# Kernel tuning notes

Hardware: AMD Instinct MI355X
Metric: run time of the kernel (lower is better)

## Reference

```python
import jax, jax.numpy as jnp
import numpy as np


def _l2norm(t, eps=1e-12):
    # matches torch F.normalize(p=2, dim=-1): x / max(||x||_2, eps)
    n = jnp.sqrt(jnp.sum(t * t, axis=-1, keepdims=True))
    return t / jnp.maximum(n, eps)


def setup_inputs() -> dict:
    key = jax.random.key(0)
    ks = jax.random.split(key, 8)
    B, N, C, H, W = 16, 4, 256, 64, 64
    d = 64  # dim_head
    x = jax.random.normal(ks[0], (B, C, H, W), jnp.float32)
    fmaps = jax.random.normal(ks[1], (B, N, C, H, W), jnp.float32)
    Wq = jax.random.normal(ks[2], (N * d, C), jnp.float32) * 0.02   # Linear [out,in]
    Wk = jax.random.normal(ks[3], (N, d, C), jnp.float32) * 0.02    # grouped 1x1 conv, per-group [d,C]
    Wv = jax.random.normal(ks[4], (N, d, C), jnp.float32) * 0.02
    rescale = jnp.ones((N, 1, 1), jnp.float32)
    Wffn = jax.random.normal(ks[5], (C, N * d), jnp.float32) * 0.02
    bffn = jnp.zeros((C,), jnp.float32)
    return {"x": x, "fmaps": fmaps, "Wq": Wq, "Wk": Wk, "Wv": Wv,
            "rescale": rescale, "Wffn": Wffn, "bffn": bffn}


def reference(x, fmaps, Wq, Wk, Wv, rescale, Wffn, bffn):
    B, N, C, H, W = fmaps.shape
    d = Wk.shape[1]
    HW = H * W

    # x: [B,C,H,W] -> tokens [B,HW,C]
    x_in = jnp.transpose(x, (0, 2, 3, 1)).reshape(B, HW, C)
    q_in = jnp.einsum('bsc,oc->bso', x_in, Wq)            # [B,HW,N*d]

    # grouped 1x1 convs on fmaps (group = fmap index n)
    fm = fmaps.reshape(B, N, C, HW)                       # [B,N,C,HW]
    k = jnp.einsum('bncs,ndc->bnds', fm, Wk)              # [B,N,d,HW]
    v = jnp.einsum('bncs,ndc->bnds', fm, Wv)              # [B,N,d,HW]

    q = jnp.transpose(q_in.reshape(B, HW, N, d), (0, 2, 3, 1))  # [B,N,d,HW]

    qn = _l2norm(q)   # normalize over spatial (HW) axis
    kn = _l2norm(k)

    attn = jnp.einsum('bnds,bnes->bnde', kn, qn) * rescale      # [B,N,d,d]
    attn = jax.nn.softmax(attn, axis=-1)
    out = jnp.einsum('bnde,bnes->bnds', attn, v)                # [B,N,d,HW]

    out = jnp.transpose(out, (0, 3, 1, 2)).reshape(B, HW, N * d)  # [B,HW,N*d]
    out = out + q_in
    out = jnp.einsum('bsi,ci->bsc', out, Wffn) + bffn + q_in      # ffn + residual
    return jnp.transpose(out.reshape(B, H, W, C), (0, 3, 1, 2))   # [B,C,H,W]
```

## Files before the change

kernel.cpp:

```cpp
#include <hip/hip_runtime.h>
#include <hip/hip_bf16.h>
#include <cmath>

using bf16 = __hip_bfloat16;
typedef __attribute__((ext_vector_type(4))) float  f32x4;
typedef __attribute__((ext_vector_type(8))) short  bf16x8;
typedef unsigned int u32;
typedef unsigned short u16;

__device__ __forceinline__ void gl_lds16(const bf16* g, bf16* l) {
    __builtin_amdgcn_global_load_lds(
        (const __attribute__((address_space(1))) u32*)g,
        (__attribute__((address_space(3))) u32*)l, 16, 0, 0);
}

__device__ __forceinline__ u32 pk2(float a, float b) {
    bf16 ha = __float2bfloat16(a), hb = __float2bfloat16(b);
    return (u32)*(u16*)&ha | ((u32)*(u16*)&hb << 16);
}
__device__ __forceinline__ float b2f(u16 v) {
    return __uint_as_float((u32)v << 16);
}

__global__ __launch_bounds__(512) void qproj8(
    const float* __restrict__ x,
    const bf16* __restrict__ Wq,
    bf16* __restrict__ qch)
{
    __shared__ __align__(16) bf16 sW[256 * 64];
    __shared__ __align__(16) bf16 sX[128 * 72];
    const int t = threadIdx.x;
    const int lane = t & 63, wid = t >> 6;
    const int wm = wid >> 1, wn = wid & 1;
    const int g = lane >> 4, lr = lane & 15;
    const int s0 = blockIdx.x * 128;
    const int b = blockIdx.y;
    const float* xb = x + (long)b * 1048576;

    f32x4 acc[4][4];
#pragma unroll
    for (int i = 0; i < 4; ++i)
#pragma unroll
        for (int j = 0; j < 4; ++j) acc[i][j] = (f32x4){0.f, 0.f, 0.f, 0.f};

    const int p  = t & 31;
    const int sl = t >> 5;

    for (int c0 = 0; c0 < 256; c0 += 64) {
        __syncthreads();
#pragma unroll
        for (int i = 0; i < 4; ++i) {
            int lin = i * 512 + t, r = lin >> 3, ch = lin & 7;
            gl_lds16(Wq + (long)r * 256 + c0 + ((ch ^ (r & 7)) << 3), &sW[lin * 8]);
        }
#pragma unroll
        for (int j = 0; j < 2; ++j) {
            int s4 = j * 16 + sl;
            const float* src = xb + (long)(c0 + 2 * p) * 4096 + s0 + s4 * 4;
            float4 a = *(const float4*)src;
            float4 bq = *(const float4*)(src + 4096);
            char* base = (char*)sX + p * 4 + (s4 * 4) * 144;
            *(u32*)(base +   0) = pk2(a.x, bq.x);
            *(u32*)(base + 144) = pk2(a.y, bq.y);
            *(u32*)(base + 288) = pk2(a.z, bq.z);
            *(u32*)(base + 432) = pk2(a.w, bq.w);
        }
        __syncthreads();
#pragma unroll
        for (int kk = 0; kk < 2; ++kk) {
            bf16x8 aw[4], fx[4];
#pragma unroll
            for (int mf = 0; mf < 4; ++mf) {
                int r = wm * 64 + mf * 16 + lr;
                aw[mf] = *(const bf16x8*)((const char*)sW + r * 128 + (((kk * 4 + g) ^ (r & 7)) << 4));
            }
#pragma unroll
            for (int nf = 0; nf < 4; ++nf) {
                int s = wn * 64 + nf * 16 + lr;
                fx[nf] = *(const bf16x8*)((const char*)sX + s * 144 + (kk * 4 + g) * 16);
            }
#pragma unroll
            for (int mf = 0; mf < 4; ++mf)
#pragma unroll
                for (int nf = 0; nf < 4; ++nf)
                    acc[mf][nf] = __builtin_amdgcn_mfma_f32_16x16x32_bf16(
                        aw[mf], fx[nf], acc[mf][nf], 0, 0, 0);
        }
    }
    bf16* qb = qch + (long)b * 1048576;
#pragma unroll
    for (int mf = 0; mf < 4; ++mf)
#pragma unroll
        for (int nf = 0; nf < 4; ++nf)
#pragma unroll
            for (int e = 0; e < 4; ++e) {
                int o = wm * 64 + mf * 16 + g * 4 + e;
                int s = s0 + wn * 64 + nf * 16 + lr;
                qb[(long)o * 4096 + s] = __float2bfloat16(acc[mf][nf][e]);
            }
}

__global__ __launch_bounds__(256) void kvproj(
    const float* __restrict__ fm,
    const bf16* __restrict__ Wk,
    const bf16* __restrict__ Wv,
    bf16* __restrict__ kb,
    bf16* __restrict__ vT)
{
    __shared__ bf16 sF[2][128 * 72];
    __shared__ bf16 sK[2][64 * 64];
    __shared__ bf16 sV[2][64 * 64];
    const int t = threadIdx.x;
    const int lane = t & 63, wid = t >> 6;
    const int g = lane >> 4, lr = lane & 15;
    const int s0 = blockIdx.x * 128;
    const int bn = blockIdx.y, n = bn & 3;
    const float* fb = fm + (long)bn * 1048576;
    const bf16* WkN = Wk + (long)n * 16384;
    const bf16* WvN = Wv + (long)n * 16384;

    f32x4 acc1[4][2];
    f32x4 acc2[2][4];
#pragma unroll
    for (int i = 0; i < 4; ++i)
#pragma unroll
        for (int j = 0; j < 2; ++j) {
            acc1[i][j] = (f32x4){0.f, 0.f, 0.f, 0.f};
            acc2[j][i] = (f32x4){0.f, 0.f, 0.f, 0.f};
        }

    const int p  = t & 31;
    const int sl = t >> 5;

    {
#pragma unroll
        for (int i = 0; i < 2; ++i) {
            int lin = i * 256 + t, r = lin >> 3, ch = lin & 7;
            int off = r * 256 + ((ch ^ (r & 7)) << 3);
            gl_lds16(WkN + off, &sK[0][lin * 8]);
            gl_lds16(WvN + off, &sV[0][lin * 8]);
        }
        float4 ra[4], rb[4];
#pragma unroll
        for (int j = 0; j < 4; ++j) {
            const float* src = fb + (long)(2 * p) * 4096 + s0 + (j * 8 + sl) * 4;
            ra[j] = *(const float4*)src;
            rb[j] = *(const float4*)(src + 4096);
        }
#pragma unroll
        for (int j = 0; j < 4; ++j) {
            char* base = (char*)&sF[0][0] + p * 4 + ((j * 8 + sl) * 4) * 144;
            *(u32*)(base +   0) = pk2(ra[j].x, rb[j].x);
            *(u32*)(base + 144) = pk2(ra[j].y, rb[j].y);
            *(u32*)(base + 288) = pk2(ra[j].z, rb[j].z);
            *(u32*)(base + 432) = pk2(ra[j].w, rb[j].w);
        }
        __syncthreads();
    }

    int cur = 0;
    for (int it = 0; it < 4; ++it) {
        const int c0n = (it + 1) * 64;
        float4 ra[4], rb[4];
        if (it < 3) {
#pragma unroll
            for (int i = 0; i < 2; ++i) {
                int lin = i * 256 + t, r = lin >> 3, ch = lin & 7;
                int off = r * 256 + c0n + ((ch ^ (r & 7)) << 3);
                gl_lds16(WkN + off, &sK[cur ^ 1][lin * 8]);
                gl_lds16(WvN + off, &sV[cur ^ 1][lin * 8]);
            }
#pragma unroll
            for (int j = 0; j < 4; ++j) {
                const float* src = fb + (long)(c0n + 2 * p) * 4096 + s0 + (j * 8 + sl) * 4;
                ra[j] = *(const float4*)src;
                rb[j] = *(const float4*)(src + 4096);
            }
        }
        const char* fbase = (const char*)&sF[cur][0];
        const char* kbase = (const char*)&sK[cur][0];
        const char* vbase = (const char*)&sV[cur][0];
#pragma unroll
        for (int kk = 0; kk < 2; ++kk) {
            bf16x8 ak[4], ff[2], bv[4];
#pragma unroll
            for (int mf = 0; mf < 4; ++mf) {
                int r = mf * 16 + lr;
                ak[mf] = *(const bf16x8*)(kbase + r * 128 + (((kk * 4 + g) ^ (r & 7)) << 4));
            }
#pragma unroll
            for (int i = 0; i < 2; ++i) {
                int s = wid * 32 + i * 16 + lr;
                ff[i] = *(const bf16x8*)(fbase + s * 144 + (kk * 4 + g) * 16);
            }
#pragma unroll
            for (int nf = 0; nf < 4; ++nf) {
                int r = nf * 16 + lr;
                bv[nf] = *(const bf16x8*)(vbase + r * 128 + (((kk * 4 + g) ^ (r & 7)) << 4));
            }
#pragma unroll
            for (int mf = 0; mf < 4; ++mf)
#pragma unroll
                for (int i = 0; i < 2; ++i)
                    acc1[mf][i] = __builtin_amdgcn_mfma_f32_16x16x32_bf16(
                        ak[mf], ff[i], acc1[mf][i], 0, 0, 0);
#pragma unroll
            for (int i = 0; i < 2; ++i)
#pragma unroll
                for (int nf = 0; nf < 4; ++nf)
                    acc2[i][nf] = __builtin_amdgcn_mfma_f32_16x16x32_bf16(
                        ff[i], bv[nf], acc2[i][nf], 0, 0, 0);
        }
        if (it < 3) {
#pragma unroll
            for (int j = 0; j < 4; ++j) {
                char* base = (char*)&sF[cur ^ 1][0] + p * 4 + ((j * 8 + sl) * 4) * 144;
                *(u32*)(base +   0) = pk2(ra[j].x, rb[j].x);
                *(u32*)(base + 144) = pk2(ra[j].y, rb[j].y);
                *(u32*)(base + 288) = pk2(ra[j].z, rb[j].z);
                *(u32*)(base + 432) = pk2(ra[j].w, rb[j].w);
            }
            __syncthreads();
            cur ^= 1;
        }
    }

    bf16* kbb = kb + (long)bn * 262144;
#pragma unroll
    for (int mf = 0; mf < 4; ++mf)
#pragma unroll
        for (int i = 0; i < 2; ++i)
#pragma unroll
            for (int e = 0; e < 4; ++e) {
                int dd = mf * 16 + g * 4 + e;
                int s  = s0 + wid * 32 + i * 16 + lr;
                kbb[(long)dd * 4096 + s] = __float2bfloat16(acc1[mf][i][e]);
            }
    bf16* vtb = vT + (long)bn * 262144;
#pragma unroll
    for (int i = 0; i < 2; ++i)
#pragma unroll
        for (int nf = 0; nf < 4; ++nf)
#pragma unroll
            for (int e = 0; e < 4; ++e) {
                int s = s0 + wid * 32 + i * 16 + g * 4 + e;
                int ec = nf * 16 + lr;
                vtb[(long)s * 64 + ec] = __float2bfloat16(acc2[i][nf][e]);
            }
}

__global__ __launch_bounds__(256) void qk_sum(
    const bf16* __restrict__ kb,
    const bf16* __restrict__ qch,
    float* __restrict__ part,
    float* __restrict__ sumq, float* __restrict__ sumk)
{
    __shared__ bf16 sA[2][64 * 64];
    __shared__ bf16 sB[2][64 * 64];
    const int t = threadIdx.x;
    const int lane = t & 63, wid = t >> 6;
    const int wm = wid >> 1, wn = wid & 1;
    const int g = lane >> 4, lr = lane & 15;
    const int ch_ = blockIdx.x;
    const int bn = blockIdx.y;
    const bf16* kbase = kb + (long)bn * 262144;
    const bf16* qbase = qch + (long)bn * 262144;

    const int srow = t >> 1;
    const int shalf = t & 1;

    f32x4 acc[2][2];
#pragma unroll
    for (int i = 0; i < 2; ++i)
#pragma unroll
        for (int j = 0; j < 2; ++j) acc[i][j] = (f32x4){0.f, 0.f, 0.f, 0.f};
    float ss = 0.f;

    {
        int k0 = ch_ * 512;
#pragma unroll
        for (int i = 0; i < 2; ++i) {
            int lin = i * 256 + t, r = lin >> 3, c = lin & 7;
            gl_lds16(kbase + (long)r * 4096 + k0 + ((c ^ (r & 7)) << 3), &sA[0][lin * 8]);
            gl_lds16(qbase + (long)r * 4096 + k0 + ((c ^ (r & 7)) << 3), &sB[0][lin * 8]);
        }
        __syncthreads();
    }

    int cur = 0;
    for (int it = 0; it < 8; ++it) {
        if (it < 7) {
            int k0 = ch_ * 512 + (it + 1) * 64;
#pragma unroll
            for (int i = 0; i < 2; ++i) {
                int lin = i * 256 + t, r = lin >> 3, c = lin & 7;
                gl_lds16(kbase + (long)r * 4096 + k0 + ((c ^ (r & 7)) << 3), &sA[cur ^ 1][lin * 8]);
                gl_lds16(qbase + (long)r * 4096 + k0 + ((c ^ (r & 7)) << 3), &sB[cur ^ 1][lin * 8]);
            }
        }
        const char* abase = (const char*)&sA[cur][0];
        const char* bbase = (const char*)&sB[cur][0];
#pragma unroll
        for (int kk = 0; kk < 2; ++kk) {
            bf16x8 af[2], bf[2];
#pragma unroll
            for (int mf = 0; mf < 2; ++mf) {
                int r = wm * 32 + mf * 16 + lr;
                af[mf] = *(const bf16x8*)(abase + r * 128 + (((kk * 4 + g) ^ (r & 7)) << 4));
            }
#pragma unroll
            for (int nf = 0; nf < 2; ++nf) {
                int r = wn * 32 + nf * 16 + lr;
                bf[nf] = *(const bf16x8*)(bbase + r * 128 + (((kk * 4 + g) ^ (r & 7)) << 4));
            }
#pragma unroll
            for (int mf = 0; mf < 2; ++mf)
#pragma unroll
                for (int nf = 0; nf < 2; ++nf)
                    acc[mf][nf] = __builtin_amdgcn_mfma_f32_16x16x32_bf16(
                        af[mf], bf[nf], acc[mf][nf], 0, 0, 0);
        }
        {
            const char* base = (srow < 64) ? abase + srow * 128
                                           : bbase + (srow - 64) * 128;
            int r7 = srow & 7;
#pragma unroll
            for (int j = 0; j < 4; ++j) {
                bf16x8 v = *(const bf16x8*)(base + (((shalf * 4 + j) ^ r7) << 4));
#pragma unroll
                for (int e = 0; e < 8; ++e) {
                    float f = b2f((u16)v[e]);
                    ss += f * f;
                }
            }
        }
        __syncthreads();
        cur ^= 1;
    }

    ss += __shfl_xor(ss, 1);
    if (shalf == 0) {
        if (srow < 64) sumk[ch_ * 4096 + bn * 64 + srow] = ss;
        else           sumq[ch_ * 4096 + bn * 64 + srow - 64] = ss;
    }
    float* pp = part + ((long)bn * 8 + ch_) * 4096;
#pragma unroll
    for (int mf = 0; mf < 2; ++mf)
#pragma unroll
        for (int nf = 0; nf < 2; ++nf)
#pragma unroll
            for (int e = 0; e < 4; ++e) {
                int m = wm * 32 + mf * 16 + g * 4 + e;
                int nn = wn * 32 + nf * 16 + lr;
                pp[m * 64 + nn] = acc[mf][nf][e];
            }
}

__global__ __launch_bounds__(256) void attn_finalize_kernel(
    const float* __restrict__ part,
    const float* __restrict__ sumq, const float* __restrict__ sumk,
    const float* __restrict__ rescale,
    bf16* __restrict__ attn_out)
{
    const int bn = blockIdx.x;
    const int n = bn & 3;
    const int t = threadIdx.x;
    const float rs = rescale[n];

    __shared__ float att[64][65];
    __shared__ float rmax[64], rsum[64];
    __shared__ float iq[64], ik[64];

    if (t < 64) {
        float s = 0.f;
#pragma unroll
        for (int c = 0; c < 8; ++c) s += sumk[c * 4096 + bn * 64 + t];
        ik[t] = 1.f / fmaxf(sqrtf(s), 1e-12f);
    } else if (t < 128) {
        float s = 0.f;
#pragma unroll
        for (int c = 0; c < 8; ++c) s += sumq[c * 4096 + bn * 64 + t - 64];
        iq[t - 64] = 1.f / fmaxf(sqrtf(s), 1e-12f);
    }
    __syncthreads();

    const float* pb = part + (size_t)bn * 8 * 4096;
#pragma unroll
    for (int p = 0; p < 16; ++p) {
        int lin = p * 256 + t;
        int dd = lin >> 6, e = lin & 63;
        float v = 0.f;
#pragma unroll
        for (int c = 0; c < 8; ++c) v += pb[c * 4096 + lin];
        v *= ik[dd] * iq[e] * rs;
        att[dd][e] = v;
    }
    __syncthreads();
    if (t < 64) {
        float m = -1e30f;
        for (int e = 0; e < 64; ++e) m = fmaxf(m, att[t][e]);
        float sm = 0.f;
        for (int e = 0; e < 64; ++e) sm += expf(att[t][e] - m);
        rmax[t] = m;
        rsum[t] = 1.0f / sm;
    }
    __syncthreads();
    bf16* ob = attn_out + (size_t)bn * 4096;
#pragma unroll
    for (int p = 0; p < 16; ++p) {
        int lin = p * 256 + t;
        int dd = lin >> 6, e = lin & 63;
        ob[lin] = __float2bfloat16(expf(att[dd][e] - rmax[dd]) * rsum[dd]);
    }
}

__global__ __launch_bounds__(256) void pvffn(
    const bf16* __restrict__ vT,
    const bf16* __restrict__ attnb,
    const bf16* __restrict__ qch,
    const bf16* __restrict__ Wf,
    const float* __restrict__ bffn,
    float* __restrict__ out)
{
    __shared__ bf16 bufA[2][8192];
    __shared__ bf16 Zs[64 * 64];
    const int t = threadIdx.x;
    const int lane = t & 63, wid = t >> 6;
    const int g = lane >> 4, lr = lane & 15;
    const int s0 = blockIdx.x * 64;
    const int b = blockIdx.y;

    f32x4 accF[4][4];
#pragma unroll
    for (int i = 0; i < 4; ++i)
#pragma unroll
        for (int j = 0; j < 4; ++j) accF[i][j] = (f32x4){0.f, 0.f, 0.f, 0.f};

    {
        const int bn = b * 4;
#pragma unroll
        for (int i = 0; i < 2; ++i) {
            int lin = i * 256 + t, r = lin >> 3, c = lin & 7;
            gl_lds16(vT + (long)bn * 262144 + (long)(s0 + r) * 64 + ((c ^ (r & 7)) << 3),
                     &bufA[0][lin * 8]);
            gl_lds16(attnb + (long)bn * 4096 + r * 64 + ((c ^ (r & 7)) << 3),
                     &bufA[0][4096 + lin * 8]);
        }
        __syncthreads();
    }

    for (int n = 0; n < 4; ++n) {
        const int bn = b * 4 + n;
        const int cur = n & 1;
        if (n < 3) {
            const int bnn = bn + 1;
#pragma unroll
            for (int i = 0; i < 2; ++i) {
                int lin = i * 256 + t, r = lin >> 3, c = lin & 7;
                gl_lds16(vT + (long)bnn * 262144 + (long)(s0 + r) * 64 + ((c ^ (r & 7)) << 3),
                         &bufA[cur ^ 1][lin * 8]);
                gl_lds16(attnb + (long)bnn * 4096 + r * 64 + ((c ^ (r & 7)) << 3),
                         &bufA[cur ^ 1][4096 + lin * 8]);
            }
        }
        bf16x8 wf[2][4];
#pragma unroll
        for (int kk = 0; kk < 2; ++kk)
#pragma unroll
            for (int mf = 0; mf < 4; ++mf)
                wf[kk][mf] = *(const bf16x8*)(
                    Wf + (long)(wid * 64 + mf * 16 + lr) * 256 + n * 64 + (kk * 4 + g) * 8);

        const char* vb = (const char*)&bufA[cur][0];
        const char* ab = vb + 8192;
        f32x4 accP[4];
#pragma unroll
        for (int j = 0; j < 4; ++j) accP[j] = (f32x4){0.f, 0.f, 0.f, 0.f};
#pragma unroll
        for (int kk = 0; kk < 2; ++kk) {
            int r = wid * 16 + lr;
            bf16x8 av = *(const bf16x8*)(vb + r * 128 + (((kk * 4 + g) ^ (r & 7)) << 4));
            bf16x8 at[4];
#pragma unroll
            for (int nf = 0; nf < 4; ++nf) {
                int rr = nf * 16 + lr;
                at[nf] = *(const bf16x8*)(ab + rr * 128 + (((kk * 4 + g) ^ (rr & 7)) << 4));
            }
#pragma unroll
            for (int nf = 0; nf < 4; ++nf)
                accP[nf] = __builtin_amdgcn_mfma_f32_16x16x32_bf16(
                    av, at[nf], accP[nf], 0, 0, 0);
        }
#pragma unroll
        for (int nf = 0; nf < 4; ++nf) {
            int slb = wid * 16 + g * 4;
            int il = nf * 16 + lr;
            ushort4 qv = *(const ushort4*)(qch + ((long)b * 256 + n * 64 + il) * 4096 + s0 + slb);
            u16 qa[4] = {qv.x, qv.y, qv.z, qv.w};
#pragma unroll
            for (int e = 0; e < 4; ++e) {
                int sl = slb + e;
                float v = accP[nf][e] + b2f(qa[e]);
                bf16 hv = __float2bfloat16(v);
                int byte = sl * 128 + ((((il >> 3) ^ (sl & 7))) << 4) + (il & 7) * 2;
                *(u16*)((char*)Zs + byte) = *(u16*)&hv;
            }
        }
        __syncthreads();
#pragma unroll
        for (int kk = 0; kk < 2; ++kk) {
            bf16x8 bz[4];
#pragma unroll
            for (int nf = 0; nf < 4; ++nf) {
                int sl = nf * 16 + lr;
                bz[nf] = *(const bf16x8*)((const char*)Zs + sl * 128 + (((kk * 4 + g) ^ (sl & 7)) << 4));
            }
#pragma unroll
            for (int mf = 0; mf < 4; ++mf)
#pragma unroll
                for (int nf = 0; nf < 4; ++nf)
                    accF[mf][nf] = __builtin_amdgcn_mfma_f32_16x16x32_bf16(
                        wf[kk][mf], bz[nf], accF[mf][nf], 0, 0, 0);
        }
        __syncthreads();
    }

    float* ob = out + (long)b * 1048576;
    const bf16* qb = qch + (long)b * 1048576;
#pragma unroll
    for (int mf = 0; mf < 4; ++mf)
#pragma unroll
        for (int e = 0; e < 4; ++e) {
            int c = wid * 64 + mf * 16 + g * 4 + e;
            float bv = bffn[c];
#pragma unroll
            for (int nf = 0; nf < 4; ++nf) {
                int s = s0 + nf * 16 + lr;
                long idx = (long)c * 4096 + s;
                ob[idx] = accF[mf][nf][e] + bv + b2f(*(const u16*)(qb + idx));
            }
        }
}

__global__ __launch_bounds__(256) void wconv(
    const float* __restrict__ a, const float* __restrict__ b,
    const float* __restrict__ c, const float* __restrict__ d,
    bf16* __restrict__ o)
{
    int i = blockIdx.x * 256 + threadIdx.x;
    int which = i >> 16, off = i & 65535;
    const float* s = (which == 0) ? a : (which == 1) ? b : (which == 2) ? c : d;
    o[i] = __float2bfloat16(s[off]);
}

extern "C" void kernel_launch(void* const* d_in, const int* in_sizes, int n_in,
                              void* d_out, int out_size, void* d_ws, size_t ws_size,
                              hipStream_t stream) {
    const float* x       = (const float*)d_in[0];
    const float* fmaps   = (const float*)d_in[1];
    const float* Wq      = (const float*)d_in[2];
    const float* Wk      = (const float*)d_in[3];
    const float* Wv      = (const float*)d_in[4];
    const float* rescale = (const float*)d_in[5];
    const float* Wffn    = (const float*)d_in[6];
    const float* bffn    = (const float*)d_in[7];
    float* out = (float*)d_out;

    char* w = (char*)d_ws;
    bf16* kbuf  = (bf16*)(w + 0);
    bf16* vT    = (bf16*)(w + 33554432L);
    bf16* qch   = (bf16*)(w + 67108864L);
    float* part = (float*)(w + 100663296L);
    bf16* attnb = (bf16*)(w + 109051904L);
    float* sumq = (float*)(w + 109576192L);
    float* sumk = (float*)(w + 109707264L);
    bf16* Wq_b  = (bf16*)(w + 109838336L);
    bf16* Wk_b  = Wq_b + 65536;
    bf16* Wv_b  = Wq_b + 131072;
    bf16* Wf_b  = Wq_b + 196608;

    dim3 blk(256);

    wconv<<<dim3(1024), blk, 0, stream>>>(Wq, Wk, Wv, Wffn, Wq_b);
    kvproj<<<dim3(32, 64), blk, 0, stream>>>(fmaps, Wk_b, Wv_b, kbuf, vT);
    qproj8<<<dim3(32, 16), dim3(512), 0, stream>>>(x, Wq_b, qch);
    qk_sum<<<dim3(8, 64), blk, 0, stream>>>(kbuf, qch, part, sumq, sumk);
    attn_finalize_kernel<<<dim3(64), blk, 0, stream>>>(part, sumq, sumk, rescale, attnb);
    pvffn<<<dim3(64, 16), blk, 0, stream>>>(vT, attnb, qch, Wf_b, bffn, out);
}
```

Measured before the change: 180.1 us.

## Fuse K/V projection with K·Q partial reduction into one kernel

```diff
diff --git a/kernel.cpp b/kernel.cpp
--- a/kernel.cpp
+++ b/kernel.cpp
@@ -100,56 +100,60 @@
             }
 }
 
-__global__ __launch_bounds__(256) void kvproj(
+__global__ __launch_bounds__(256) void kvqk2(
     const float* __restrict__ fm,
     const bf16* __restrict__ Wk,
     const bf16* __restrict__ Wv,
-    bf16* __restrict__ kb,
-    bf16* __restrict__ vT)
+    const bf16* __restrict__ qch,
+    bf16* __restrict__ vT,
+    float* __restrict__ part,
+    float* __restrict__ sumq, float* __restrict__ sumk)
 {
-    __shared__ bf16 sF[2][128 * 72];
-    __shared__ bf16 sK[2][64 * 64];
-    __shared__ bf16 sV[2][64 * 64];
+    __shared__ __align__(16) char smem[69632];
+
     const int t = threadIdx.x;
     const int lane = t & 63, wid = t >> 6;
     const int g = lane >> 4, lr = lane & 15;
-    const int s0 = blockIdx.x * 128;
+    const int ch_ = blockIdx.x;
     const int bn = blockIdx.y, n = bn & 3;
     const float* fb = fm + (long)bn * 1048576;
     const bf16* WkN = Wk + (long)n * 16384;
     const bf16* WvN = Wv + (long)n * 16384;
-
-    f32x4 acc1[4][2];
-    f32x4 acc2[2][4];
-#pragma unroll
-    for (int i = 0; i < 4; ++i)
-#pragma unroll
-        for (int j = 0; j < 2; ++j) {
-            acc1[i][j] = (f32x4){0.f, 0.f, 0.f, 0.f};
-            acc2[j][i] = (f32x4){0.f, 0.f, 0.f, 0.f};
-        }
+    const bf16* qbase = qch + (long)bn * 262144;
+    bf16* vtb = vT + (long)bn * 262144;
 
     const int p  = t & 31;
     const int sl = t >> 5;
+
+    f32x4 accQ[4];
+#pragma unroll
+    for (int i = 0; i < 4; ++i) accQ[i] = (f32x4){0.f, 0.f, 0.f, 0.f};
+    float kss[4][4];
+#pragma unroll
+    for (int i = 0; i < 4; ++i)
+#pragma unroll
+        for (int j = 0; j < 4; ++j) kss[i][j] = 0.f;
+    float qss[4] = {0.f, 0.f, 0.f, 0.f};
 
     {
 #pragma unroll
         for (int i = 0; i < 2; ++i) {
             int lin = i * 256 + t, r = lin >> 3, ch = lin & 7;
             int off = r * 256 + ((ch ^ (r & 7)) << 3);
-            gl_lds16(WkN + off, &sK[0][lin * 8]);
-            gl_lds16(WvN + off, &sV[0][lin * 8]);
-        }
+            gl_lds16(WkN + off, (bf16*)(smem + 36864) + lin * 8);
+            gl_lds16(WvN + off, (bf16*)(smem + 53248) + lin * 8);
+        }
+        const int ss0 = ch_ * 512;
         float4 ra[4], rb[4];
 #pragma unroll
         for (int j = 0; j < 4; ++j) {
-            const float* src = fb + (long)(2 * p) * 4096 + s0 + (j * 8 + sl) * 4;
+            const float* src = fb + (long)(2 * p) * 4096 + ss0 + (j * 8 + sl) * 4;
             ra[j] = *(const float4*)src;
             rb[j] = *(const float4*)(src + 4096);
         }
 #pragma unroll
         for (int j = 0; j < 4; ++j) {
-            char* base = (char*)&sF[0][0] + p * 4 + ((j * 8 + sl) * 4) * 144;
+            char* base = smem + p * 4 + ((j * 8 + sl) * 4) * 144;
             *(u32*)(base +   0) = pk2(ra[j].x, rb[j].x);
             *(u32*)(base + 144) = pk2(ra[j].y, rb[j].y);
             *(u32*)(base + 288) = pk2(ra[j].z, rb[j].z);
@@ -158,202 +162,196 @@
         __syncthreads();
     }
 
-    int cur = 0;
-    for (int it = 0; it < 4; ++it) {
-        const int c0n = (it + 1) * 64;
-        float4 ra[4], rb[4];
-        if (it < 3) {
+    int fcur = 0, wcur = 0;
+    f32x4 acc1[4][2], acc2[2][4];
+
+    for (int fi = 0; fi < 16; ++fi) {
+        const int c = fi & 3;
+        if (c == 0) {
+#pragma unroll
+            for (int i = 0; i < 4; ++i)
+#pragma unroll
+                for (int j = 0; j < 2; ++j) {
+                    acc1[i][j] = (f32x4){0.f, 0.f, 0.f, 0.f};
+                    acc2[j][i] = (f32x4){0.f, 0.f, 0.f, 0.f};
+                }
+        }
+        const bool havF = (fi < 15);
+        if (c < 3) {
+            char* kw = (wcur ? smem + 36864 : smem + 45056);
+            char* vw = (wcur ? smem + 53248 : smem + 61440);
 #pragma unroll
             for (int i = 0; i < 2; ++i) {
                 int lin = i * 256 + t, r = lin >> 3, ch = lin & 7;
-                int off = r * 256 + c0n + ((ch ^ (r & 7)) << 3);
-                gl_lds16(WkN + off, &sK[cur ^ 1][lin * 8]);
-                gl_lds16(WvN + off, &sV[cur ^ 1][lin * 8]);
-            }
+                int off = r * 256 + (c + 1) * 64 + ((ch ^ (r & 7)) << 3);
+                gl_lds16(WkN + off, (bf16*)kw + lin * 8);
+                gl_lds16(WvN + off, (bf16*)vw + lin * 8);
+            }
+        }
+        float4 ra[4], rb[4];
+        if (havF) {
+            const int nss0 = ch_ * 512 + ((fi + 1) >> 2) * 128;
+            const int nc0  = ((fi + 1) & 3) * 64;
 #pragma unroll
             for (int j = 0; j < 4; ++j) {
-                const float* src = fb + (long)(c0n + 2 * p) * 4096 + s0 + (j * 8 + sl) * 4;
+                const float* src = fb + (long)(nc0 + 2 * p) * 4096 + nss0 + (j * 8 + sl) * 4;
                 ra[j] = *(const float4*)src;
                 rb[j] = *(const float4*)(src + 4096);
             }
         }
-        const char* fbase = (const char*)&sF[cur][0];
-        const char* kbase = (const char*)&sK[cur][0];
-        const char* vbase = (const char*)&sV[cur][0];
-#pragma unroll
-        for (int kk = 0; kk < 2; ++kk) {
-            bf16x8 ak[4], ff[2], bv[4];
-#pragma unroll
-            for (int mf = 0; mf < 4; ++mf) {
-                int r = mf * 16 + lr;
-                ak[mf] = *(const bf16x8*)(kbase + r * 128 + (((kk * 4 + g) ^ (r & 7)) << 4));
-            }
-#pragma unroll
-            for (int i = 0; i < 2; ++i) {
-                int s = wid * 32 + i * 16 + lr;
-                ff[i] = *(const bf16x8*)(fbase + s * 144 + (kk * 4 + g) * 16);
-            }
-#pragma unroll
-            for (int nf = 0; nf < 4; ++nf) {
-                int r = nf * 16 + lr;
-                bv[nf] = *(const bf16x8*)(vbase + r * 128 + (((kk * 4 + g) ^ (r & 7)) << 4));
-            }
-#pragma unroll
-            for (int mf = 0; mf < 4; ++mf)
+        {
+            const char* fbase = smem + (fcur ? 18432 : 0);
+            const char* kbase = smem + (wcur ? 45056 : 36864);
+            const char* vbase = smem + (wcur ? 61440 : 53248);
+#pragma unroll
+            for (int kk = 0; kk < 2; ++kk) {
+                bf16x8 ak[4], ff[2], bv[4];
+#pragma unroll
+                for (int mf = 0; mf < 4; ++mf) {
+                    int r = mf * 16 + lr;
+                    ak[mf] = *(const bf16x8*)(kbase + r * 128 + (((kk * 4 + g) ^ (r & 7)) << 4));
+                }
+#pragma unroll
+                for (int i = 0; i < 2; ++i) {
+                    int s = wid * 32 + i * 16 + lr;
+                    ff[i] = *(const bf16x8*)(fbase + s * 144 + (kk * 4 + g) * 16);
+                }
+#pragma unroll
+                for (int nf = 0; nf < 4; ++nf) {
+                    int r = nf * 16 + lr;
+                    bv[nf] = *(const bf16x8*)(vbase + r * 128 + (((kk * 4 + g) ^ (r & 7)) << 4));
+                }
+#pragma unroll
+                for (int mf = 0; mf < 4; ++mf)
+#pragma unroll
+                    for (int i = 0; i < 2; ++i)
+                        acc1[mf][i] = __builtin_amdgcn_mfma_f32_16x16x32_bf16(
+                            ak[mf], ff[i], acc1[mf][i], 0, 0, 0);
 #pragma unroll
                 for (int i = 0; i < 2; ++i)
-                    acc1[mf][i] = __builtin_amdgcn_mfma_f32_16x16x32_bf16(
-                        ak[mf], ff[i], acc1[mf][i], 0, 0, 0);
-#pragma unroll
-            for (int i = 0; i < 2; ++i)
-#pragma unroll
-                for (int nf = 0; nf < 4; ++nf)
-                    acc2[i][nf] = __builtin_amdgcn_mfma_f32_16x16x32_bf16(
-                        ff[i], bv[nf], acc2[i][nf], 0, 0, 0);
-        }
-        if (it < 3) {
+#pragma unroll
+                    for (int nf = 0; nf < 4; ++nf)
+                        acc2[i][nf] = __builtin_amdgcn_mfma_f32_16x16x32_bf16(
+                            ff[i], bv[nf], acc2[i][nf], 0, 0, 0);
+            }
+        }
+        if (havF) {
+            char* nb = smem + (fcur ? 0 : 18432);
 #pragma unroll
             for (int j = 0; j < 4; ++j) {
-                char* base = (char*)&sF[cur ^ 1][0] + p * 4 + ((j * 8 + sl) * 4) * 144;
+                char* base = nb + p * 4 + ((j * 8 + sl) * 4) * 144;
                 *(u32*)(base +   0) = pk2(ra[j].x, rb[j].x);
                 *(u32*)(base + 144) = pk2(ra[j].y, rb[j].y);
                 *(u32*)(base + 288) = pk2(ra[j].z, rb[j].z);
                 *(u32*)(base + 432) = pk2(ra[j].w, rb[j].w);
             }
             __syncthreads();
-            cur ^= 1;
-        }
-    }
-
-    bf16* kbb = kb + (long)bn * 262144;
-#pragma unroll
-    for (int mf = 0; mf < 4; ++mf)
-#pragma unroll
-        for (int i = 0; i < 2; ++i)
+            fcur ^= 1;
+        }
+        if (c < 3) wcur ^= 1;
+
+        if (c == 3) {
+            const int sub = fi >> 2;
+            const int ss0 = ch_ * 512 + sub * 128;
+            const int ovl = wcur ^ 1;
+            char* ktA = smem + (ovl ? 45056 : 36864);
+            char* ktB = smem + (ovl ? 61440 : 53248);
+#pragma unroll
+            for (int mf = 0; mf < 4; ++mf)
+#pragma unroll
+                for (int i = 0; i < 2; ++i)
+#pragma unroll
+                    for (int e = 0; e < 4; ++e) {
+                        int dd = mf * 16 + g * 4 + e;
+                        int sc = wid * 32 + i * 16 + lr;
+                        float f = acc1[mf][i][e];
+                        kss[mf][e] += f * f;
+                        bf16 hv = __float2bfloat16(f);
+                        char* base = (dd < 32) ? ktA : ktB;
+                        int byte = (dd & 31) * 256 + ((((sc >> 3) ^ (dd & 7))) << 4) + (sc & 7) * 2;
+                        *(u16*)(base + byte) = *(u16*)&hv;
+                    }
+            if (sub < 3) {
+                char* kw = (wcur ? smem + 45056 : smem + 36864);
+                char* vw = (wcur ? smem + 61440 : smem + 53248);
+#pragma unroll
+                for (int i = 0; i < 2; ++i) {
+                    int lin = i * 256 + t, r = lin >> 3, ch = lin & 7;
+                    int off = r * 256 + ((ch ^ (r & 7)) << 3);
+                    gl_lds16(WkN + off, (bf16*)kw + lin * 8);
+                    gl_lds16(WvN + off, (bf16*)vw + lin * 8);
+                }
+            }
+            __syncthreads();
+#pragma unroll
+            for (int kks = 0; kks < 4; ++kks) {
+                int rA = wid * 16 + lr;
+                const char* kt = (wid < 2) ? ktA : ktB;
+                bf16x8 af = *(const bf16x8*)(kt + (rA & 31) * 256 + (((kks * 4 + g) ^ (rA & 7)) << 4));
+                bf16x8 bq[4];
+#pragma unroll
+                for (int nf = 0; nf < 4; ++nf) {
+                    int rB = nf * 16 + lr;
+                    bq[nf] = *(const bf16x8*)(qbase + (long)rB * 4096 + ss0 + (kks * 4 + g) * 8);
+                }
+#pragma unroll
+                for (int nf = 0; nf < 4; ++nf) {
+                    accQ[nf] = __builtin_amdgcn_mfma_f32_16x16x32_bf16(
+                        af, bq[nf], accQ[nf], 0, 0, 0);
+#pragma unroll
+                    for (int e2 = 0; e2 < 8; ++e2) {
+                        float f = b2f((u16)bq[nf][e2]);
+                        qss[nf] += f * f;
+                    }
+                }
+            }
+#pragma unroll
+            for (int i = 0; i < 2; ++i)
+#pragma unroll
+                for (int nf = 0; nf < 4; ++nf)
+#pragma unroll
+                    for (int e = 0; e < 4; ++e) {
+                        int s = ss0 + wid * 32 + i * 16 + g * 4 + e;
+                        vtb[(long)s * 64 + nf * 16 + lr] = __float2bfloat16(acc2[i][nf][e]);
+                    }
+            __syncthreads();
+        }
+    }
+
+    float* pp = part + ((long)bn * 8 + ch_) * 4096;
+#pragma unroll
+    for (int nf = 0; nf < 4; ++nf)
+#pragma unroll
+        for (int e = 0; e < 4; ++e) {
+            int dd = wid * 16 + g * 4 + e;
+            pp[dd * 64 + nf * 16 + lr] = accQ[nf][e];
+        }
+    {
+        float* red = (float*)smem;
+#pragma unroll
+        for (int mf = 0; mf < 4; ++mf)
 #pragma unroll
             for (int e = 0; e < 4; ++e) {
-                int dd = mf * 16 + g * 4 + e;
-                int s  = s0 + wid * 32 + i * 16 + lr;
-                kbb[(long)dd * 4096 + s] = __float2bfloat16(acc1[mf][i][e]);
-            }
-    bf16* vtb = vT + (long)bn * 262144;
-#pragma unroll
-    for (int i = 0; i < 2; ++i)
-#pragma unroll
-        for (int nf = 0; nf < 4; ++nf)
-#pragma unroll
-            for (int e = 0; e < 4; ++e) {
-                int s = s0 + wid * 32 + i * 16 + g * 4 + e;
-                int ec = nf * 16 + lr;
-                vtb[(long)s * 64 + ec] = __float2bfloat16(acc2[i][nf][e]);
-            }
-}
-
-__global__ __launch_bounds__(256) void qk_sum(
-    const bf16* __restrict__ kb,
-    const bf16* __restrict__ qch,
-    float* __restrict__ part,
-    float* __restrict__ sumq, float* __restrict__ sumk)
-{
-    __shared__ bf16 sA[2][64 * 64];
-    __shared__ bf16 sB[2][64 * 64];
-    const int t = threadIdx.x;
-    const int lane = t & 63, wid = t >> 6;
-    const int wm = wid >> 1, wn = wid & 1;
-    const int g = lane >> 4, lr = lane & 15;
-    const int ch_ = blockIdx.x;
-    const int bn = blockIdx.y;
-    const bf16* kbase = kb + (long)bn * 262144;
-    const bf16* qbase = qch + (long)bn * 262144;
-
-    const int srow = t >> 1;
-    const int shalf = t & 1;
-
-    f32x4 acc[2][2];
-#pragma unroll
-    for (int i = 0; i < 2; ++i)
-#pragma unroll
-        for (int j = 0; j < 2; ++j) acc[i][j] = (f32x4){0.f, 0.f, 0.f, 0.f};
-    float ss = 0.f;
-
-    {
-        int k0 = ch_ * 512;
-#pragma unroll
-        for (int i = 0; i < 2; ++i) {
-            int lin = i * 256 + t, r = lin >> 3, c = lin & 7;
-            gl_lds16(kbase + (long)r * 4096 + k0 + ((c ^ (r & 7)) << 3), &sA[0][lin * 8]);
-            gl_lds16(qbase + (long)r * 4096 + k0 + ((c ^ (r & 7)) << 3), &sB[0][lin * 8]);
-        }
-        __syncthreads();
-    }
-
-    int cur = 0;
-    for (int it = 0; it < 8; ++it) {
-        if (it < 7) {
-            int k0 = ch_ * 512 + (it + 1) * 64;
-#pragma unroll
-            for (int i = 0; i < 2; ++i) {
-                int lin = i * 256 + t, r = lin >> 3, c = lin & 7;
-                gl_lds16(kbase + (long)r * 4096 + k0 + ((c ^ (r & 7)) << 3), &sA[cur ^ 1][lin * 8]);
-                gl_lds16(qbase + (long)r * 4096 + k0 + ((c ^ (r & 7)) << 3), &sB[cur ^ 1][lin * 8]);
-            }
-        }
-        const char* abase = (const char*)&sA[cur][0];
-        const char* bbase = (const char*)&sB[cur][0];
-#pragma unroll
-        for (int kk = 0; kk < 2; ++kk) {
-            bf16x8 af[2], bf[2];
-#pragma unroll
-            for (int mf = 0; mf < 2; ++mf) {
-                int r = wm * 32 + mf * 16 + lr;
-                af[mf] = *(const bf16x8*)(abase + r * 128 + (((kk * 4 + g) ^ (r & 7)) << 4));
-            }
-#pragma unroll
-            for (int nf = 0; nf < 2; ++nf) {
-                int r = wn * 32 + nf * 16 + lr;
-                bf[nf] = *(const bf16x8*)(bbase + r * 128 + (((kk * 4 + g) ^ (r & 7)) << 4));
-            }
-#pragma unroll
-            for (int mf = 0; mf < 2; ++mf)
-#pragma unroll
-                for (int nf = 0; nf < 2; ++nf)
-                    acc[mf][nf] = __builtin_amdgcn_mfma_f32_16x16x32_bf16(
-                        af[mf], bf[nf], acc[mf][nf], 0, 0, 0);
-        }
-        {
-            const char* base = (srow < 64) ? abase + srow * 128
-                                           : bbase + (srow - 64) * 128;
-            int r7 = srow & 7;
-#pragma unroll
-            for (int j = 0; j < 4; ++j) {
-                bf16x8 v = *(const bf16x8*)(base + (((shalf * 4 + j) ^ r7) << 4));
-#pragma unroll
-                for (int e = 0; e < 8; ++e) {
-                    float f = b2f((u16)v[e]);
-                    ss += f * f;
-                }
-            }
-        }
-        __syncthreads();
-        cur ^= 1;
-    }
-
-    ss += __shfl_xor(ss, 1);
-    if (shalf == 0) {
-        if (srow < 64) sumk[ch_ * 4096 + bn * 64 + srow] = ss;
-        else           sumq[ch_ * 4096 + bn * 64 + srow - 64] = ss;
-    }
-    float* pp = part + ((long)bn * 8 + ch_) * 4096;
-#pragma unroll
-    for (int mf = 0; mf < 2; ++mf)
-#pragma unroll
-        for (int nf = 0; nf < 2; ++nf)
-#pragma unroll
-            for (int e = 0; e < 4; ++e) {
-                int m = wm * 32 + mf * 16 + g * 4 + e;
-                int nn = wn * 32 + nf * 16 + lr;
-                pp[m * 64 + nn] = acc[mf][nf][e];
-            }
+                float v = kss[mf][e];
+                v += __shfl_xor(v, 1);
+                v += __shfl_xor(v, 2);
+                v += __shfl_xor(v, 4);
+                v += __shfl_xor(v, 8);
+                if (lr == 0) red[wid * 64 + mf * 16 + g * 4 + e] = v;
+            }
+        __syncthreads();
+        if (t < 64)
+            sumk[ch_ * 4096 + bn * 64 + t] =
+                red[t] + red[64 + t] + red[128 + t] + red[192 + t];
+    }
+#pragma unroll
+    for (int nf = 0; nf < 4; ++nf) {
+        float v = qss[nf];
+        v += __shfl_xor(v, 16);
+        v += __shfl_xor(v, 32);
+        if (wid == 0 && g == 0)
+            sumq[ch_ * 4096 + bn * 64 + nf * 16 + lr] = v;
+    }
 }
 
 __global__ __launch_bounds__(256) void attn_finalize_kernel(
@@ -567,7 +565,6 @@
     float* out = (float*)d_out;
 
     char* w = (char*)d_ws;
-    bf16* kbuf  = (bf16*)(w + 0);
     bf16* vT    = (bf16*)(w + 33554432L);
     bf16* qch   = (bf16*)(w + 67108864L);
     float* part = (float*)(w + 100663296L);
@@ -582,9 +579,8 @@
     dim3 blk(256);
 
     wconv<<<dim3(1024), blk, 0, stream>>>(Wq, Wk, Wv, Wffn, Wq_b);
-    kvproj<<<dim3(32, 64), blk, 0, stream>>>(fmaps, Wk_b, Wv_b, kbuf, vT);
     qproj8<<<dim3(32, 16), dim3(512), 0, stream>>>(x, Wq_b, qch);
-    qk_sum<<<dim3(8, 64), blk, 0, stream>>>(kbuf, qch, part, sumq, sumk);
+    kvqk2<<<dim3(8, 64), blk, 0, stream>>>(fmaps, Wk_b, Wv_b, qch, vT, part, sumq, sumk);
     attn_finalize_kernel<<<dim3(64), blk, 0, stream>>>(part, sumq, sumk, rescale, attnb);
     pvffn<<<dim3(64, 16), blk, 0, stream>>>(vT, attnb, qch, Wf_b, bffn, out);
 }
```

Measured after the change: 227.1 us. +26.1%, slower.
